# Kernel optimization log

Measured on AMD Instinct MI355X. Metric: run time of the kernel, lower is better.

## Reference

```python
import jax, jax.numpy as jnp
import numpy as np

L = 0.05  # lx = ly = lz box half-extent

# 8 box corners [8,3]
_CORNERS = jnp.array([[sx * L, sy * L, sz * L]
                      for sx in (-1.0, 1.0) for sy in (-1.0, 1.0) for sz in (-1.0, 1.0)],
                     dtype=jnp.float32)
# match original ordering: [-,-,-],[-,-,+],[-,+,-],... which the comprehension above yields


def _euler_R(pose):
    """pose: [B,6] -> R [B,3,3], t [B,3] (yaw, pitch, roll convention from source)."""
    yaw, pitch, roll = pose[:, 0], pose[:, 1], pose[:, 2]
    cy, sy = jnp.cos(yaw), jnp.sin(yaw)
    cp, sp = jnp.cos(pitch), jnp.sin(pitch)
    cr, sr = jnp.cos(roll), jnp.sin(roll)
    R = jnp.stack([
        jnp.stack([cy * cp, cy * sp * sr - sy * cr, cy * sp * cr + sy * sr], axis=-1),
        jnp.stack([sy * cp, sy * sp * sr + cy * cr, sy * sp * cr - cy * sr], axis=-1),
        jnp.stack([-sp, cp * sr, cp * cr], axis=-1),
    ], axis=-2)  # [B,3,3]
    t = pose[:, 3:]  # [B,3]
    return R, t


def _transform_corners(pose):
    R, t = _euler_R(pose)
    # [B,8,3] = corners @ R^T + t
    return jnp.einsum('bij,nj->bni', R, _CORNERS) + t[:, None, :]


def setup_inputs() -> dict:
    key = jax.random.key(0)
    k1, k2, k3, k4 = jax.random.split(key, 4)
    B, C = 1048576, 16
    return {
        'pred_pose': jax.random.normal(k1, (B, 6), dtype=jnp.float32),
        'pred_class': jax.random.normal(k2, (B, C), dtype=jnp.float32),
        'target_pose': jax.random.normal(k3, (B, 6), dtype=jnp.float32),
        'target_class': jax.random.normal(k4, (B, C), dtype=jnp.float32),
    }


def reference(pred_pose, pred_class, target_pose, target_class):
    pts_pred = _transform_corners(pred_pose)    # [B,8,3]
    pts_gt = _transform_corners(target_pose)    # [B,8,3]
    # per-sample pose diff: mean over 8 corner L2 norms, then mean over batch
    norms = jnp.linalg.norm(pts_pred - pts_gt, axis=-1)  # [B,8]
    loss_pose = norms.mean(axis=-1).mean()
    class_loss = jnp.mean((pred_class - target_class) ** 2)
    total_loss = loss_pose + class_loss
    return total_loss, loss_pose, class_loss
```

## Files before the change

### kernel.cpp

```cpp
#include <hip/hip_runtime.h>
#include <math.h>

#define CORNER_L 0.05f

__device__ __forceinline__ void euler_R(float yaw, float pitch, float roll, float R[9]) {
    float cy, sy, cp, sp, cr, sr;
    __sincosf(yaw,   &sy, &cy);
    __sincosf(pitch, &sp, &cp);
    __sincosf(roll,  &sr, &cr);
    R[0] = cy * cp;
    R[1] = cy * sp * sr - sy * cr;
    R[2] = cy * sp * cr + sy * sr;
    R[3] = sy * cp;
    R[4] = sy * sp * sr + cy * cr;
    R[5] = sy * sp * cr - cy * sr;
    R[6] = -sp;
    R[7] = cp * sr;
    R[8] = cp * cr;
}

__global__ __launch_bounds__(256) void pose_loss_reduce(
    const float* __restrict__ pred_pose,
    const float* __restrict__ pred_class,
    const float* __restrict__ target_pose,
    const float* __restrict__ target_class,
    float* __restrict__ ws, int B)
{
    const int tid    = blockIdx.x * blockDim.x + threadIdx.x;
    const int stride = gridDim.x * blockDim.x;

    float pose_acc  = 0.0f;
    float class_acc = 0.0f;

    const float4* __restrict__ pc4 = (const float4*)pred_class;
    const float4* __restrict__ tc4 = (const float4*)target_class;

    for (int i = tid; i < B; i += stride) {
        #pragma unroll
        for (int k = 0; k < 4; ++k) {
            float4 p = pc4[(size_t)i * 4 + k];
            float4 t = tc4[(size_t)i * 4 + k];
            float dx = p.x - t.x, dy = p.y - t.y, dz = p.z - t.z, dw = p.w - t.w;
            class_acc += dx * dx + dy * dy + dz * dz + dw * dw;
        }

        const float* pp = pred_pose   + (size_t)i * 6;
        const float* tp = target_pose + (size_t)i * 6;
        float Rp[9], Rg[9];
        euler_R(pp[0], pp[1], pp[2], Rp);
        euler_R(tp[0], tp[1], tp[2], Rg);
        float dtx = pp[3] - tp[3];
        float dty = pp[4] - tp[4];
        float dtz = pp[5] - tp[5];

        float a0 = CORNER_L * (Rp[0] - Rg[0]), a1 = CORNER_L * (Rp[1] - Rg[1]), a2 = CORNER_L * (Rp[2] - Rg[2]);
        float b0 = CORNER_L * (Rp[3] - Rg[3]), b1 = CORNER_L * (Rp[4] - Rg[4]), b2 = CORNER_L * (Rp[5] - Rg[5]);
        float c0 = CORNER_L * (Rp[6] - Rg[6]), c1 = CORNER_L * (Rp[7] - Rg[7]), c2 = CORNER_L * (Rp[8] - Rg[8]);

        float nsum = 0.0f;
        #pragma unroll
        for (int s = 0; s < 8; ++s) {
            float sx = (s & 4) ? 1.0f : -1.0f;
            float sy = (s & 2) ? 1.0f : -1.0f;
            float sz = (s & 1) ? 1.0f : -1.0f;
            float d0 = sx * a0 + sy * a1 + sz * a2 + dtx;
            float d1 = sx * b0 + sy * b1 + sz * b2 + dty;
            float d2 = sx * c0 + sy * c1 + sz * c2 + dtz;
            nsum += sqrtf(d0 * d0 + d1 * d1 + d2 * d2);
        }
        pose_acc += nsum;
    }

    #pragma unroll
    for (int off = 32; off > 0; off >>= 1) {
        pose_acc  += __shfl_down(pose_acc,  off);
        class_acc += __shfl_down(class_acc, off);
    }

    __shared__ float s_pose[4], s_class[4];
    const int lane = threadIdx.x & 63;
    const int wave = threadIdx.x >> 6;
    if (lane == 0) { s_pose[wave] = pose_acc; s_class[wave] = class_acc; }
    __syncthreads();
    if (threadIdx.x == 0) {
        float ps = s_pose[0] + s_pose[1] + s_pose[2] + s_pose[3];
        float cs = s_class[0] + s_class[1] + s_class[2] + s_class[3];
        atomicAdd(&ws[0], ps);
        atomicAdd(&ws[1], cs);
    }
}

__global__ void pose_loss_finalize(const float* __restrict__ ws,
                                   float* __restrict__ out,
                                   float inv_pose, float inv_class)
{
    if (threadIdx.x == 0 && blockIdx.x == 0) {
        float lp = ws[0] * inv_pose;
        float lc = ws[1] * inv_class;
        out[0] = lp + lc;
        out[1] = lp;
        out[2] = lc;
    }
}

extern "C" void kernel_launch(void* const* d_in, const int* in_sizes, int n_in,
                              void* d_out, int out_size, void* d_ws, size_t ws_size,
                              hipStream_t stream) {
    const float* pred_pose    = (const float*)d_in[0];
    const float* pred_class   = (const float*)d_in[1];
    const float* target_pose  = (const float*)d_in[2];
    const float* target_class = (const float*)d_in[3];
    float* out = (float*)d_out;
    float* ws  = (float*)d_ws;

    const int B = in_sizes[0] / 6;

    hipMemsetAsync(ws, 0, 2 * sizeof(float), stream);

    const int block = 256;
    const int grid  = 2048;
    pose_loss_reduce<<<grid, block, 0, stream>>>(pred_pose, pred_class,
                                                 target_pose, target_class, ws, B);

    const float inv_pose  = 1.0f / (8.0f  * (float)B);
    const float inv_class = 1.0f / (16.0f * (float)B);
    pose_loss_finalize<<<1, 64, 0, stream>>>(ws, out, inv_pose, inv_class);
}
```

Baseline: 197.8 us.

## Stage pose arrays through shared memory with coalesced float4 loads, drop atomics

```diff
diff --git a/kernel.cpp b/kernel.cpp
--- a/kernel.cpp
+++ b/kernel.cpp
@@ -2,6 +2,9 @@
 #include <math.h>
 
 #define CORNER_L 0.05f
+
+constexpr int THREADS = 256;
+constexpr int BLOCKS  = 1024;
 
 __device__ __forceinline__ void euler_R(float yaw, float pitch, float roll, float R[9]) {
     float cy, sy, cp, sp, cr, sr;
@@ -19,56 +22,95 @@
     R[8] = cp * cr;
 }
 
-__global__ __launch_bounds__(256) void pose_loss_reduce(
-    const float* __restrict__ pred_pose,
-    const float* __restrict__ pred_class,
-    const float* __restrict__ target_pose,
-    const float* __restrict__ target_class,
+__device__ __forceinline__ float pose_elem(
+    float py, float pp_, float pr, float ptx, float pty, float ptz,
+    float ty, float tp_, float tr, float ttx, float tty, float ttz)
+{
+    float Rp[9], Rg[9];
+    euler_R(py, pp_, pr, Rp);
+    euler_R(ty, tp_, tr, Rg);
+    float dtx = ptx - ttx;
+    float dty = pty - tty;
+    float dtz = ptz - ttz;
+
+    float a0 = CORNER_L * (Rp[0] - Rg[0]), a1 = CORNER_L * (Rp[1] - Rg[1]), a2 = CORNER_L * (Rp[2] - Rg[2]);
+    float b0 = CORNER_L * (Rp[3] - Rg[3]), b1 = CORNER_L * (Rp[4] - Rg[4]), b2 = CORNER_L * (Rp[5] - Rg[5]);
+    float c0 = CORNER_L * (Rp[6] - Rg[6]), c1 = CORNER_L * (Rp[7] - Rg[7]), c2 = CORNER_L * (Rp[8] - Rg[8]);
+
+    float nsum = 0.0f;
+    #pragma unroll
+    for (int s = 0; s < 8; ++s) {
+        float sx = (s & 4) ? 1.0f : -1.0f;
+        float sy = (s & 2) ? 1.0f : -1.0f;
+        float sz = (s & 1) ? 1.0f : -1.0f;
+        float d0 = sx * a0 + sy * a1 + sz * a2 + dtx;
+        float d1 = sx * b0 + sy * b1 + sz * b2 + dty;
+        float d2 = sx * c0 + sy * c1 + sz * c2 + dtz;
+        nsum += sqrtf(d0 * d0 + d1 * d1 + d2 * d2);
+    }
+    return nsum;
+}
+
+__global__ __launch_bounds__(THREADS, 4) void pose_loss_reduce(
+    const float4* __restrict__ pp4,
+    const float4* __restrict__ pc4,
+    const float4* __restrict__ tp4,
+    const float4* __restrict__ tc4,
     float* __restrict__ ws, int B)
 {
-    const int tid    = blockIdx.x * blockDim.x + threadIdx.x;
-    const int stride = gridDim.x * blockDim.x;
+    __shared__ float s_p[3072];
+    __shared__ float s_t[3072];
 
-    float pose_acc  = 0.0f;
-    float class_acc = 0.0f;
+    const int tid = threadIdx.x;
+    const int elems_per_blk = B / gridDim.x;
+    const int elem_base = blockIdx.x * elems_per_blk;
 
-    const float4* __restrict__ pc4 = (const float4*)pred_class;
-    const float4* __restrict__ tc4 = (const float4*)target_class;
+    float class_acc0 = 0.0f, class_acc1 = 0.0f;
+    float pose_acc = 0.0f;
 
-    for (int i = tid; i < B; i += stride) {
+    {
+        const int n4 = elems_per_blk * 4;
+        const size_t base = (size_t)elem_base * 4;
+        #pragma unroll 4
+        for (int k = tid; k < n4; k += 2 * THREADS) {
+            float4 p0 = pc4[base + k];
+            float4 t0 = tc4[base + k];
+            float4 p1 = pc4[base + k + THREADS];
+            float4 t1 = tc4[base + k + THREADS];
+            float dx0 = p0.x - t0.x, dy0 = p0.y - t0.y, dz0 = p0.z - t0.z, dw0 = p0.w - t0.w;
+            float dx1 = p1.x - t1.x, dy1 = p1.y - t1.y, dz1 = p1.z - t1.z, dw1 = p1.w - t1.w;
+            class_acc0 += dx0 * dx0 + dy0 * dy0 + dz0 * dz0 + dw0 * dw0;
+            class_acc1 += dx1 * dx1 + dy1 * dy1 + dz1 * dz1 + dw1 * dw1;
+        }
+    }
+    float class_acc = class_acc0 + class_acc1;
+
+    const int sub_elems = elems_per_blk / 2;
+    float4* sp4 = (float4*)s_p;
+    float4* st4 = (float4*)s_t;
+    for (int sc = 0; sc < 2; ++sc) {
+        const int ebase = elem_base + sc * sub_elems;
+        const int nf4 = sub_elems * 6 / 4;
+        const size_t gbase = (size_t)ebase * 6 / 4;
         #pragma unroll
-        for (int k = 0; k < 4; ++k) {
-            float4 p = pc4[(size_t)i * 4 + k];
-            float4 t = tc4[(size_t)i * 4 + k];
-            float dx = p.x - t.x, dy = p.y - t.y, dz = p.z - t.z, dw = p.w - t.w;
-            class_acc += dx * dx + dy * dy + dz * dz + dw * dw;
+        for (int k = tid; k < 768; k += THREADS) {
+            sp4[k] = pp4[gbase + k];
+            st4[k] = tp4[gbase + k];
         }
-
-        const float* pp = pred_pose   + (size_t)i * 6;
-        const float* tp = target_pose + (size_t)i * 6;
-        float Rp[9], Rg[9];
-        euler_R(pp[0], pp[1], pp[2], Rp);
-        euler_R(tp[0], tp[1], tp[2], Rg);
-        float dtx = pp[3] - tp[3];
-        float dty = pp[4] - tp[4];
-        float dtz = pp[5] - tp[5];
-
-        float a0 = CORNER_L * (Rp[0] - Rg[0]), a1 = CORNER_L * (Rp[1] - Rg[1]), a2 = CORNER_L * (Rp[2] - Rg[2]);
-        float b0 = CORNER_L * (Rp[3] - Rg[3]), b1 = CORNER_L * (Rp[4] - Rg[4]), b2 = CORNER_L * (Rp[5] - Rg[5]);
-        float c0 = CORNER_L * (Rp[6] - Rg[6]), c1 = CORNER_L * (Rp[7] - Rg[7]), c2 = CORNER_L * (Rp[8] - Rg[8]);
-
-        float nsum = 0.0f;
-        #pragma unroll
-        for (int s = 0; s < 8; ++s) {
-            float sx = (s & 4) ? 1.0f : -1.0f;
-            float sy = (s & 2) ? 1.0f : -1.0f;
-            float sz = (s & 1) ? 1.0f : -1.0f;
-            float d0 = sx * a0 + sy * a1 + sz * a2 + dtx;
-            float d1 = sx * b0 + sy * b1 + sz * b2 + dty;
-            float d2 = sx * c0 + sy * c1 + sz * c2 + dtz;
-            nsum += sqrtf(d0 * d0 + d1 * d1 + d2 * d2);
+        __syncthreads();
+        {
+            float4 A  = sp4[tid * 3 + 0];
+            float4 Bv = sp4[tid * 3 + 1];
+            float4 Cv = sp4[tid * 3 + 2];
+            float4 D  = st4[tid * 3 + 0];
+            float4 E  = st4[tid * 3 + 1];
+            float4 F  = st4[tid * 3 + 2];
+            pose_acc += pose_elem(A.x, A.y, A.z, A.w, Bv.x, Bv.y,
+                                  D.x, D.y, D.z, D.w, E.x, E.y);
+            pose_acc += pose_elem(Bv.z, Bv.w, Cv.x, Cv.y, Cv.z, Cv.w,
+                                  E.z, E.w, F.x, F.y, F.z, F.w);
         }
-        pose_acc += nsum;
+        __syncthreads();
     }
 
     #pragma unroll
@@ -76,27 +118,39 @@
         pose_acc  += __shfl_down(pose_acc,  off);
         class_acc += __shfl_down(class_acc, off);
     }
-
-    __shared__ float s_pose[4], s_class[4];
-    const int lane = threadIdx.x & 63;
-    const int wave = threadIdx.x >> 6;
-    if (lane == 0) { s_pose[wave] = pose_acc; s_class[wave] = class_acc; }
+    __shared__ float r_pose[4], r_class[4];
+    const int lane = tid & 63;
+    const int wave = tid >> 6;
+    if (lane == 0) { r_pose[wave] = pose_acc; r_class[wave] = class_acc; }
     __syncthreads();
-    if (threadIdx.x == 0) {
-        float ps = s_pose[0] + s_pose[1] + s_pose[2] + s_pose[3];
-        float cs = s_class[0] + s_class[1] + s_class[2] + s_class[3];
-        atomicAdd(&ws[0], ps);
-        atomicAdd(&ws[1], cs);
+    if (tid == 0) {
+        ws[blockIdx.x]             = r_pose[0] + r_pose[1] + r_pose[2] + r_pose[3];
+        ws[gridDim.x + blockIdx.x] = r_class[0] + r_class[1] + r_class[2] + r_class[3];
     }
 }
 
-__global__ void pose_loss_finalize(const float* __restrict__ ws,
-                                   float* __restrict__ out,
-                                   float inv_pose, float inv_class)
+__global__ __launch_bounds__(THREADS) void pose_loss_finalize(
+    const float* __restrict__ ws, float* __restrict__ out,
+    int nblocks, float inv_pose, float inv_class)
 {
-    if (threadIdx.x == 0 && blockIdx.x == 0) {
-        float lp = ws[0] * inv_pose;
-        float lc = ws[1] * inv_class;
+    float p = 0.0f, c = 0.0f;
+    for (int k = threadIdx.x; k < nblocks; k += THREADS) {
+        p += ws[k];
+        c += ws[nblocks + k];
+    }
+    #pragma unroll
+    for (int off = 32; off > 0; off >>= 1) {
+        p += __shfl_down(p, off);
+        c += __shfl_down(c, off);
+    }
+    __shared__ float r_p[4], r_c[4];
+    const int lane = threadIdx.x & 63;
+    const int wave = threadIdx.x >> 6;
+    if (lane == 0) { r_p[wave] = p; r_c[wave] = c; }
+    __syncthreads();
+    if (threadIdx.x == 0) {
+        float lp = (r_p[0] + r_p[1] + r_p[2] + r_p[3]) * inv_pose;
+        float lc = (r_c[0] + r_c[1] + r_c[2] + r_c[3]) * inv_class;
         out[0] = lp + lc;
         out[1] = lp;
         out[2] = lc;
@@ -106,23 +160,19 @@
 extern "C" void kernel_launch(void* const* d_in, const int* in_sizes, int n_in,
                               void* d_out, int out_size, void* d_ws, size_t ws_size,
                               hipStream_t stream) {
-    const float* pred_pose    = (const float*)d_in[0];
-    const float* pred_class   = (const float*)d_in[1];
-    const float* target_pose  = (const float*)d_in[2];
-    const float* target_class = (const float*)d_in[3];
+    const float4* pred_pose    = (const float4*)d_in[0];
+    const float4* pred_class   = (const float4*)d_in[1];
+    const float4* target_pose  = (const float4*)d_in[2];
+    const float4* target_class = (const float4*)d_in[3];
     float* out = (float*)d_out;
     float* ws  = (float*)d_ws;
 
     const int B = in_sizes[0] / 6;
 
-    hipMemsetAsync(ws, 0, 2 * sizeof(float), stream);
-
-    const int block = 256;
-    const int grid  = 2048;
-    pose_loss_reduce<<<grid, block, 0, stream>>>(pred_pose, pred_class,
-                                                 target_pose, target_class, ws, B);
+    pose_loss_reduce<<<BLOCKS, THREADS, 0, stream>>>(pred_pose, pred_class,
+                                                     target_pose, target_class, ws, B);
 
     const float inv_pose  = 1.0f / (8.0f  * (float)B);
     const float inv_class = 1.0f / (16.0f * (float)B);
-    pose_loss_finalize<<<1, 64, 0, stream>>>(ws, out, inv_pose, inv_class);
+    pose_loss_finalize<<<1, THREADS, 0, stream>>>(ws, out, BLOCKS, inv_pose, inv_class);
 }
```

After: 197.6 us. No clear change (-0.1%).
